# Kernel optimization log

Hardware: AMD Instinct MI355X
Metric: run time of the kernel (lower is better)

The kernel has to match this reference:

```python
import jax, jax.numpy as jnp
import numpy as np

EPS = 1e-7  # K.epsilon()
NUM_ROUTING = 3


def squash(v, axis=-1):
    s = jnp.sum(jnp.square(v), axis=axis, keepdims=True)
    scale = s / (1.0 + s) / jnp.sqrt(s + EPS)
    return scale * v


def setup_inputs() -> dict:
    key = jax.random.key(0)
    k1, k2 = jax.random.split(key)
    B, I, D = 256, 2048, 8      # batch, input_num_capsule, input_dim_capsule
    J, E = 10, 16               # num_capsule, dim_capsule
    inputs = jax.random.normal(k1, (B, I, D), dtype=jnp.float32)
    # glorot-uniform-ish init for W [J, I, E, D]
    limit = np.sqrt(6.0 / (D + E)).astype(np.float32)
    W = jax.random.uniform(k2, (J, I, E, D), dtype=jnp.float32, minval=-limit, maxval=limit)
    return {"inputs": inputs, "W": W}


def reference(inputs, W):
    # u_hat[b,j,i,e] = W[j,i] @ u[b,i]  -> [B, J, I, E]
    u_hat = jnp.einsum('bid,jied->bjie', inputs, W)
    u_hat_stop = jax.lax.stop_gradient(u_hat)
    B, J, I, E = u_hat.shape
    b = jnp.zeros((B, J, I), dtype=u_hat.dtype)
    for i in range(NUM_ROUTING):
        # faithful to tf.nn.softmax(b, dim=1): softmax over num_capsule axis
        c = jax.nn.softmax(b, axis=1)
        if i == NUM_ROUTING - 1:
            outputs = squash(jnp.einsum('bji,bjie->bje', c, u_hat))
        else:
            outputs = squash(jnp.einsum('bji,bjie->bje', c, u_hat_stop))
            b = b + jnp.einsum('bje,bjie->bji', outputs, u_hat_stop)
    # concat along last axis: [B, J, E + I]
    return jnp.concatenate([outputs, c], axis=-1)
```

## Files before the change

### kernel.cpp

```cpp
#include <hip/hip_runtime.h>
#include <math.h>

#define II 2048
#define BB 256
#define JJ 10
#define ICH 16
#define ICHUNKS (II/ICH)
#define SJE (BB*JJ*16)
#define CPAD 20

typedef __attribute__((address_space(3))) unsigned lds_u32;
typedef __attribute__((address_space(1))) const unsigned glb_u32;
typedef _Float16 h4 __attribute__((ext_vector_type(4)));
typedef _Float16 h8 __attribute__((ext_vector_type(8)));
typedef __attribute__((ext_vector_type(4))) float f32x4;

__device__ __forceinline__ void gload16(const void* g, void* l) {
  __builtin_amdgcn_global_load_lds((glb_u32*)g, (lds_u32*)l, 16, 0, 0);
}

template<int N>
__device__ __forceinline__ float rrot16(float v) {
  const int i = __float_as_int(v);
  return __int_as_float(__builtin_amdgcn_update_dpp(i, i, 0x120 + N, 0xF, 0xF, false));
}
__device__ __forceinline__ float rsum16(float v) {
  v += rrot16<8>(v); v += rrot16<4>(v); v += rrot16<2>(v); v += rrot16<1>(v);
  return v;
}
__device__ __forceinline__ float xor16swz(float v) {
  return __int_as_float(__builtin_amdgcn_ds_swizzle(__float_as_int(v), 0x401F));
}

#define XF4 (BB * II * 8 / 4)
#define WF4 (JJ * II * 128 / 4)
__global__ __launch_bounds__(256)
void prep_half(const float* __restrict__ x, const float* __restrict__ W,
               _Float16* __restrict__ xh, _Float16* __restrict__ wh) {
  for (int s = blockIdx.x * 256 + threadIdx.x; s < XF4 + WF4; s += gridDim.x * 256) {
    const float4 v = (s < XF4) ? *reinterpret_cast<const float4*>(x + (size_t)s * 4)
                               : *reinterpret_cast<const float4*>(W + (size_t)(s - XF4) * 4);
    h4 o; o.x = (_Float16)v.x; o.y = (_Float16)v.y; o.z = (_Float16)v.z; o.w = (_Float16)v.w;
    _Float16* dst = (s < XF4) ? (xh + (size_t)s * 4) : (wh + (size_t)(s - XF4) * 4);
    *reinterpret_cast<h4*>(dst) = o;
  }
}

__global__ __launch_bounds__(256)
void pass0_mfma(const _Float16* __restrict__ xh, const _Float16* __restrict__ wh,
                float* __restrict__ part) {
  const int t = threadIdx.x, wid = t >> 6, lane = t & 63;
  const int lg = lane >> 4, lm = lane & 15;
  const int chunk = blockIdx.x * 4 + wid;
  const int mb = blockIdx.y * 16;
  f32x4 acc0 = {0,0,0,0}, acc1 = {0,0,0,0}, acc2 = {0,0,0,0}, acc3 = {0,0,0,0};
  f32x4 acc4_ = {0,0,0,0}, acc5 = {0,0,0,0}, acc6 = {0,0,0,0}, acc7 = {0,0,0,0};
  f32x4 acc8 = {0,0,0,0}, acc9 = {0,0,0,0};
  const int ibase = chunk * 16;
#pragma unroll
  for (int ks = 0; ks < 4; ++ks) {
    const int i = ibase + ks * 4 + lg;
    const h8 a = *reinterpret_cast<const h8*>(xh + ((size_t)(mb + lm) * II + i) * 8);
#define MM(J, ACC)                                                              \
    {                                                                           \
      const h8 bv = *reinterpret_cast<const h8*>(                               \
          wh + (((size_t)(J) * II + i) * 16 + lm) * 8);                         \
      ACC = __builtin_amdgcn_mfma_f32_16x16x32_f16(a, bv, ACC, 0, 0, 0);        \
    }
    MM(0, acc0) MM(1, acc1) MM(2, acc2) MM(3, acc3) MM(4, acc4_)
    MM(5, acc5) MM(6, acc6) MM(7, acc7) MM(8, acc8) MM(9, acc9)
#undef MM
  }
  float* base = part + (size_t)chunk * SJE;
#define ST(J, ACC)                                                        \
  {                                                                       \
    _Pragma("unroll")                                                     \
    for (int r = 0; r < 4; ++r)                                           \
      base[((size_t)(mb + lg * 4 + r) * JJ + (J)) * 16 + lm] = ACC[r];    \
  }
  ST(0, acc0) ST(1, acc1) ST(2, acc2) ST(3, acc3) ST(4, acc4_)
  ST(5, acc5) ST(6, acc6) ST(7, acc7) ST(8, acc8) ST(9, acc9)
#undef ST
}

template<int PASS>
__global__ __launch_bounds__(128, 1)
void routing_mfma(const _Float16* __restrict__ xh, const _Float16* __restrict__ wh,
                  const float* __restrict__ o_eff, float* __restrict__ part,
                  float* __restrict__ out) {
  __shared__ __align__(16) float s_acc[16 * 164];
  __shared__ _Float16 c_tile[(PASS == 2) ? (16 * JJ * CPAD) : 4];

  const int t = threadIdx.x;
  const int w = t >> 6;
  const int lane = t & 63;
  const int lm = lane & 15;
  const int eg = lane >> 4;
  const int ic = blockIdx.x;
  const int b0 = blockIdx.y * 16;
  const int b = b0 + lm;
  const int i0 = ic * ICH;

  float4 o[JJ];
#pragma unroll
  for (int j = 0; j < JJ; ++j)
    o[j] = *reinterpret_cast<const float4*>(
        o_eff + ((size_t)b * JJ + j) * 16 + eg * 4);

  f32x4 acc[JJ];
#pragma unroll
  for (int j = 0; j < JJ; ++j) acc[j] = f32x4{0.f, 0.f, 0.f, 0.f};

  const f32x4 z4 = {0.f, 0.f, 0.f, 0.f};
  h8 xfrag = {0, 0, 0, 0, 0, 0, 0, 0};
  h8 wf[JJ];
#pragma unroll
  for (int j = 0; j < JJ; ++j) wf[j] = h8{0, 0, 0, 0, 0, 0, 0, 0};

  const _Float16* xrow = xh + (size_t)b * II * 8;
  const int ibeg = i0 + w * (ICH / 2);

  if (lane < 16) {
    xfrag = *reinterpret_cast<const h8*>(xrow + (size_t)ibeg * 8);
#pragma unroll
    for (int j = 0; j < JJ; ++j)
      wf[j] = *reinterpret_cast<const h8*>(
          wh + (((size_t)j * II + ibeg) * 16 + lm) * 8);
  }

#pragma unroll 1
  for (int ii = 0; ii < ICH / 2; ++ii) {
    const int i = ibeg + ii;
    const int il = w * (ICH / 2) + ii;
    const int inext = (ii + 1 < ICH / 2) ? (i + 1) : i;

    f32x4 uh[JJ];
#pragma unroll
    for (int j = 0; j < JJ; ++j) {
      uh[j] = __builtin_amdgcn_mfma_f32_16x16x32_f16(wf[j], xfrag, z4, 0, 0, 0);
      if (lane < 16)
        wf[j] = *reinterpret_cast<const h8*>(
            wh + (((size_t)j * II + inext) * 16 + lm) * 8);
    }
    if (lane < 16)
      xfrag = *reinterpret_cast<const h8*>(xrow + (size_t)inext * 8);

    float cj[JJ];
    float D = 0.f;
#pragma unroll
    for (int j = 0; j < JJ; ++j) {
      float v = o[j].x * uh[j][0];
      v = fmaf(o[j].y, uh[j][1], v);
      v = fmaf(o[j].z, uh[j][2], v);
      v = fmaf(o[j].w, uh[j][3], v);
      v += xor16swz(v);
      v += __shfl_xor(v, 32);
      const float pp = __expf(v);
      cj[j] = pp;
      D += pp;
    }
    const float rD = __builtin_amdgcn_rcpf(D);
#pragma unroll
    for (int j = 0; j < JJ; ++j) {
      const float c = cj[j] * rD;
      cj[j] = c;
      acc[j][0] = fmaf(c, uh[j][0], acc[j][0]);
      acc[j][1] = fmaf(c, uh[j][1], acc[j][1]);
      acc[j][2] = fmaf(c, uh[j][2], acc[j][2]);
      acc[j][3] = fmaf(c, uh[j][3], acc[j][3]);
    }
    if (PASS == 2) {
#pragma unroll
      for (int j = 0; j < JJ; ++j) {
        const int owner = (j >= 9) ? 3 : (j / 3);
        if (eg == owner)
          c_tile[(lm * JJ + j) * CPAD + il] = (_Float16)cj[j];
      }
    }
  }

  if (w == 0) {
#pragma unroll
    for (int j = 0; j < JJ; ++j)
      *reinterpret_cast<f32x4*>(&s_acc[lm * 164 + j * 16 + eg * 4]) = acc[j];
  }
  __syncthreads();
  if (w == 1) {
#pragma unroll
    for (int j = 0; j < JJ; ++j) {
      f32x4 v = *reinterpret_cast<const f32x4*>(&s_acc[lm * 164 + j * 16 + eg * 4]);
      v += acc[j];
      *reinterpret_cast<f32x4*>(
          part + (size_t)ic * SJE + ((size_t)b * JJ + j) * 16 + eg * 4) = v;
    }
  }

  if (PASS == 2) {
    for (int s = t; s < 16 * JJ * (ICH / 4); s += 128) {
      const int row = s >> 2, q = s & 3;
      const int bb = row / JJ, jj = row - bb * JJ;
      const h4 cv = *reinterpret_cast<const h4*>(&c_tile[row * CPAD + q * 4]);
      float4 ov;
      ov.x = (float)cv.x; ov.y = (float)cv.y; ov.z = (float)cv.z; ov.w = (float)cv.w;
      *reinterpret_cast<float4*>(
          out + ((size_t)(b0 + bb) * JJ + jj) * 2064 + 16 + i0 + q * 4) = ov;
    }
  }
}

__global__ __launch_bounds__(256)
void finish_pass(const float* __restrict__ part, float* __restrict__ o_eff,
                 float* __restrict__ out, int pass) {
  const int idx = blockIdx.x * 256 + threadIdx.x;
  float a = 0.f;
#pragma unroll 8
  for (int k = 0; k < ICHUNKS; ++k) a += part[(size_t)k * SJE + idx];
  if (pass == 0) a *= 0.1f;
  const float s2 = rsum16(a * a);
  const float scale = s2 / ((1.f + s2) * sqrtf(s2 + 1e-7f));
  const float v = scale * a;
  if (pass == 0) o_eff[idx] = v;
  else if (pass == 1) o_eff[idx] += v;
  else out[(size_t)(idx >> 4) * 2064 + (idx & 15)] = v;
}

#define BBLK 32
#define NBW 8
template<int PASS>
__global__ __launch_bounds__(256, 1)
void routing_pass_atomic(const float* __restrict__ x, const float* __restrict__ W,
                         const float* __restrict__ o_eff, float* __restrict__ sdst,
                         float* __restrict__ out) {
  __shared__ __align__(16) float x_lds[BBLK * ICH * 8];
  __shared__ _Float16 c_tile[(PASS == 2) ? (BBLK * JJ * 18) : 4];

  const int t = threadIdx.x;
  const int wid = t >> 6;
  const int lane = t & 63;
  const int eg = lane >> 4;
  const int j = lane & 15;
  const int jv = (j < JJ);
  const int jr = jv ? j : 0;
  const int ic = blockIdx.x;
  const int b0 = blockIdx.y * BBLK;
  const int bw = __builtin_amdgcn_readfirstlane(b0 + wid * NBW);
  const int i0 = ic * ICH;
  const float* wbase = W + ((size_t)jr * II + i0) * 128 + eg * 32;

  float4 o4[NBW];
  if (PASS > 0) {
#pragma unroll
    for (int nb = 0; nb < NBW; ++nb)
      o4[nb] = *reinterpret_cast<const float4*>(
          o_eff + ((size_t)(bw + nb) * JJ + jr) * 16 + eg * 4);
  }
  float4 acc4[NBW];
#pragma unroll
  for (int nb = 0; nb < NBW; ++nb) acc4[nb] = make_float4(0.f, 0.f, 0.f, 0.f);

#pragma unroll
  for (int k = 0; k < 4; ++k) {
    const int s = k * 256 + t;
    const int bl = s >> 5, rem = s & 31, il = rem >> 1, h = rem & 1;
    gload16(x + ((size_t)(b0 + bl) * II + i0 + il) * 8 + h * 4,
            &x_lds[(k * 256 + wid * 64) * 4]);
  }
  __syncthreads();

#pragma unroll 1
  for (int il = 0; il < ICH; ++il) {
    const float* wp = wbase + il * 128;
    float4 wv[8];
#pragma unroll
    for (int r = 0; r < 8; ++r)
      wv[r] = *reinterpret_cast<const float4*>(wp + r * 4);
#pragma unroll
    for (int nb = 0; nb < NBW; ++nb) {
      const float* xp = &x_lds[((wid * NBW + nb) * ICH + il) * 8];
      const float4 xa = *reinterpret_cast<const float4*>(xp);
      const float4 xb = *reinterpret_cast<const float4*>(xp + 4);
#define DOT8F(q, dst)                                  \
      float dst = wv[2*(q)].x * xa.x;                  \
      dst = fmaf(wv[2*(q)].y, xa.y, dst);              \
      dst = fmaf(wv[2*(q)].z, xa.z, dst);              \
      dst = fmaf(wv[2*(q)].w, xa.w, dst);              \
      dst = fmaf(wv[2*(q)+1].x, xb.x, dst);            \
      dst = fmaf(wv[2*(q)+1].y, xb.y, dst);            \
      dst = fmaf(wv[2*(q)+1].z, xb.z, dst);            \
      dst = fmaf(wv[2*(q)+1].w, xb.w, dst);
      DOT8F(0, u0) DOT8F(1, u1) DOT8F(2, u2) DOT8F(3, u3)
#undef DOT8F
      float c;
      if (PASS == 0) {
        c = 0.1f;
      } else {
        float lp = o4[nb].x * u0;
        lp = fmaf(o4[nb].y, u1, lp);
        lp = fmaf(o4[nb].z, u2, lp);
        lp = fmaf(o4[nb].w, u3, lp);
        lp += xor16swz(lp);
        lp += __shfl_xor(lp, 32);
        const float pp = jv ? __expf(lp) : 0.f;
        const float su = rsum16(pp);
        c = pp * __builtin_amdgcn_rcpf(su);
      }
      acc4[nb].x = fmaf(c, u0, acc4[nb].x);
      acc4[nb].y = fmaf(c, u1, acc4[nb].y);
      acc4[nb].z = fmaf(c, u2, acc4[nb].z);
      acc4[nb].w = fmaf(c, u3, acc4[nb].w);
      if (PASS == 2) {
        if (eg == 0 && jv)
          c_tile[((wid * NBW + nb) * JJ + j) * 18 + il] = (_Float16)c;
      }
    }
  }

  if (PASS == 2) {
    __syncthreads();
    for (int s = t; s < BBLK * JJ * ICH; s += 256) {
      const int row = s >> 4, col = s & 15;
      const int bb = row / 10, jj = row - bb * 10;
      out[((size_t)(b0 + bb) * JJ + jj) * 2064 + 16 + i0 + col] =
          (float)c_tile[row * 18 + col];
    }
  }

  if (jv) {
#pragma unroll
    for (int nb = 0; nb < NBW; ++nb) {
      float* sp = sdst + ((size_t)(bw + nb) * JJ + j) * 16 + eg * 4;
      atomicAdd(&sp[0], acc4[nb].x);
      atomicAdd(&sp[1], acc4[nb].y);
      atomicAdd(&sp[2], acc4[nb].z);
      atomicAdd(&sp[3], acc4[nb].w);
    }
  }
}

__global__ __launch_bounds__(256)
void squash_update(const float* __restrict__ s, float* __restrict__ o_eff,
                   float* __restrict__ out, int pass) {
  const int idx = blockIdx.x * blockDim.x + threadIdx.x;
  if (idx >= BB * JJ) return;
  const float* sp = s + (size_t)idx * 16;
  const float pre = (pass == 0) ? 0.1f : 1.f;
  float v[16];
  float s2 = 0.f;
#pragma unroll
  for (int e = 0; e < 16; ++e) { v[e] = pre * sp[e]; s2 = fmaf(v[e], v[e], s2); }
  const float scale = s2 / ((1.f + s2) * sqrtf(s2 + 1e-7f));
  if (pass == 0) {
    float* op = o_eff + (size_t)idx * 16;
#pragma unroll
    for (int e = 0; e < 16; ++e) op[e] = scale * v[e];
  } else if (pass == 1) {
    float* op = o_eff + (size_t)idx * 16;
#pragma unroll
    for (int e = 0; e < 16; ++e) op[e] += scale * v[e];
  } else {
    float* dst = out + (size_t)idx * 2064;
#pragma unroll
    for (int e = 0; e < 16; ++e) dst[e] = scale * v[e];
  }
}

extern "C" void kernel_launch(void* const* d_in, const int* in_sizes, int n_in,
                              void* d_out, int out_size, void* d_ws, size_t ws_size,
                              hipStream_t stream) {
  const float* x = (const float*)d_in[0];
  const float* W = (const float*)d_in[1];
  float* out = (float*)d_out;
  float* ws = (float*)d_ws;

  const size_t part_f = (size_t)ICHUNKS * SJE;
  const size_t xh_f   = (size_t)BB * II * 8 / 2;
  const size_t wh_f   = (size_t)JJ * II * 128 / 2;
  const size_t need = (part_f + SJE + xh_f + wh_f) * sizeof(float);

  if (ws_size >= need) {
    float* part = ws;
    float* oe   = ws + part_f;
    _Float16* xh = (_Float16*)(ws + part_f + SJE);
    _Float16* wh = (_Float16*)(ws + part_f + SJE + xh_f);
    prep_half<<<2048, 256, 0, stream>>>(x, W, xh, wh);
    pass0_mfma<<<dim3(32, 16), 256, 0, stream>>>(xh, wh, part);
    finish_pass<<<SJE / 256, 256, 0, stream>>>(part, oe, out, 0);
    routing_mfma<1><<<dim3(ICHUNKS, 16), 128, 0, stream>>>(xh, wh, oe, part, nullptr);
    finish_pass<<<SJE / 256, 256, 0, stream>>>(part, oe, out, 1);
    routing_mfma<2><<<dim3(ICHUNKS, 16), 128, 0, stream>>>(xh, wh, oe, part, out);
    finish_pass<<<SJE / 256, 256, 0, stream>>>(part, oe, out, 2);
  } else {
    float* s0 = ws;
    float* s1 = ws + SJE;
    float* s2 = ws + 2 * SJE;
    float* oe = ws + 3 * SJE;
    hipMemsetAsync(ws, 0, (size_t)4 * SJE * sizeof(float), stream);
    routing_pass_atomic<0><<<dim3(ICHUNKS, BB / BBLK), 256, 0, stream>>>(x, W, nullptr, s0, nullptr);
    squash_update<<<10, 256, 0, stream>>>(s0, oe, out, 0);
    routing_pass_atomic<1><<<dim3(ICHUNKS, BB / BBLK), 256, 0, stream>>>(x, W, oe, s1, nullptr);
    squash_update<<<10, 256, 0, stream>>>(s1, oe, out, 1);
    routing_pass_atomic<2><<<dim3(ICHUNKS, BB / BBLK), 256, 0, stream>>>(x, W, oe, s2, out);
    squash_update<<<10, 256, 0, stream>>>(s2, oe, out, 2);
  }
}
```

Measured before the change: 132.1 us.

## Software-pipeline MFMA step against softmax/accumulate of previous capsule

Restructures the per-input-capsule loop into a two-stage software pipeline: the MFMA computing u_hat and the partial agreement logits for step i+1 is issued before the cross-lane reduction, exp, normalization and accumulation of step i. The aim is to hide MFMA and load latency behind VALU/shuffle work. u_hat is kept in fp16 between stages to save registers, which loses precision in the weighted sum. The softmax denominator is also summed as a tree instead of a serial chain.

```diff
diff --git a/kernel.cpp b/kernel.cpp
--- a/kernel.cpp
+++ b/kernel.cpp
@@ -118,7 +118,7 @@
   for (int j = 0; j < JJ; ++j) wf[j] = h8{0, 0, 0, 0, 0, 0, 0, 0};
 
   const _Float16* xrow = xh + (size_t)b * II * 8;
-  const int ibeg = i0 + w * (ICH / 2);
+  const int ibeg = i0 + w * 8;
 
   if (lane < 16) {
     xfrag = *reinterpret_cast<const h8*>(xrow + (size_t)ibeg * 8);
@@ -128,56 +128,76 @@
           wh + (((size_t)j * II + ibeg) * 16 + lm) * 8);
   }
 
+  float lgA[JJ], lgB[JJ];
+  h4 upA[JJ], upB[JJ];
+
+#define MSTEP(LG, UP, INEXT)                                                  \
+  {                                                                           \
+    const int inx_ = (INEXT);                                                 \
+    _Pragma("unroll")                                                         \
+    for (int j = 0; j < JJ; ++j) {                                            \
+      const f32x4 uh_ =                                                       \
+          __builtin_amdgcn_mfma_f32_16x16x32_f16(wf[j], xfrag, z4, 0, 0, 0);  \
+      if (lane < 16)                    \
+        wf[j] = *reinterpret_cast<const h8*>(                                 \
+            wh + (((size_t)j * II + inx_) * 16 + lm) * 8);                    \
+      float v_ = o[j].x * uh_[0];                                             \
+      v_ = fmaf(o[j].y, uh_[1], v_);                                          \
+      v_ = fmaf(o[j].z, uh_[2], v_);                                          \
+      v_ = fmaf(o[j].w, uh_[3], v_);                                          \
+      LG[j] = v_;                                                             \
+      h4 u_;                                                                  \
+      u_.x = (_Float16)uh_[0]; u_.y = (_Float16)uh_[1];                       \
+      u_.z = (_Float16)uh_[2]; u_.w = (_Float16)uh_[3];                       \
+      UP[j] = u_;                                                             \
+    }                                                                         \
+    if (lane < 16)               \
+      xfrag = *reinterpret_cast<const h8*>(xrow + (size_t)inx_ * 8);          \
+  }
+
+#define SSTEP(LG, UP, IL)                                                     \
+  {                                                                           \
+    float p_[JJ];                                                             \
+    _Pragma("unroll")                                                         \
+    for (int j = 0; j < JJ; ++j) {                                            \
+      float v_ = LG[j];                                                       \
+      v_ += xor16swz(v_);                                                     \
+      v_ += __shfl_xor(v_, 32);                                               \
+      p_[j] = __expf(v_);          \
+    }                                                                         \
+    const float d01_ = p_[0] + p_[1], d23_ = p_[2] + p_[3];                   \
+    const float d45_ = p_[4] + p_[5], d67_ = p_[6] + p_[7];                   \
+    const float d89_ = p_[8] + p_[9];                                         \
+    const float D_ = (d01_ + d23_) + (d45_ + d67_) + d89_;                    \
+    const float rD_ = __builtin_amdgcn_rcpf(D_);                              \
+    _Pragma("unroll")                                                         \
+    for (int j = 0; j < JJ; ++j) {                                            \
+      const float c_ = p_[j] * rD_;                                           \
+      acc[j][0] = fmaf(c_, (float)UP[j].x, acc[j][0]);                        \
+      acc[j][1] = fmaf(c_, (float)UP[j].y, acc[j][1]);                        \
+      acc[j][2] = fmaf(c_, (float)UP[j].z, acc[j][2]);                        \
+      acc[j][3] = fmaf(c_, (float)UP[j].w, acc[j][3]);                        \
+      if (PASS == 2) {                                                        \
+        const int owner_ = (j >= 9) ? 3 : (j / 3);                            \
+        if (eg == owner_)                                                     \
+          c_tile[(lm * JJ + j) * CPAD + (IL)] = (_Float16)c_;                 \
+      }                                                                       \
+    }                                                                         \
+  }
+
+  MSTEP(lgA, upA, ibeg + 1)
 #pragma unroll 1
-  for (int ii = 0; ii < ICH / 2; ++ii) {
-    const int i = ibeg + ii;
-    const int il = w * (ICH / 2) + ii;
-    const int inext = (ii + 1 < ICH / 2) ? (i + 1) : i;
-
-    f32x4 uh[JJ];
-#pragma unroll
-    for (int j = 0; j < JJ; ++j) {
-      uh[j] = __builtin_amdgcn_mfma_f32_16x16x32_f16(wf[j], xfrag, z4, 0, 0, 0);
-      if (lane < 16)
-        wf[j] = *reinterpret_cast<const h8*>(
-            wh + (((size_t)j * II + inext) * 16 + lm) * 8);
-    }
-    if (lane < 16)
-      xfrag = *reinterpret_cast<const h8*>(xrow + (size_t)inext * 8);
-
-    float cj[JJ];
-    float D = 0.f;
-#pragma unroll
-    for (int j = 0; j < JJ; ++j) {
-      float v = o[j].x * uh[j][0];
-      v = fmaf(o[j].y, uh[j][1], v);
-      v = fmaf(o[j].z, uh[j][2], v);
-      v = fmaf(o[j].w, uh[j][3], v);
-      v += xor16swz(v);
-      v += __shfl_xor(v, 32);
-      const float pp = __expf(v);
-      cj[j] = pp;
-      D += pp;
-    }
-    const float rD = __builtin_amdgcn_rcpf(D);
-#pragma unroll
-    for (int j = 0; j < JJ; ++j) {
-      const float c = cj[j] * rD;
-      cj[j] = c;
-      acc[j][0] = fmaf(c, uh[j][0], acc[j][0]);
-      acc[j][1] = fmaf(c, uh[j][1], acc[j][1]);
-      acc[j][2] = fmaf(c, uh[j][2], acc[j][2]);
-      acc[j][3] = fmaf(c, uh[j][3], acc[j][3]);
-    }
-    if (PASS == 2) {
-#pragma unroll
-      for (int j = 0; j < JJ; ++j) {
-        const int owner = (j >= 9) ? 3 : (j / 3);
-        if (eg == owner)
-          c_tile[(lm * JJ + j) * CPAD + il] = (_Float16)cj[j];
-      }
-    }
-  }
+  for (int k = 0; k < 3; ++k) {
+    MSTEP(lgB, upB, ibeg + 2 * k + 2)
+    SSTEP(lgA, upA, w * 8 + 2 * k)
+    MSTEP(lgA, upA, ibeg + 2 * k + 3)
+    SSTEP(lgB, upB, w * 8 + 2 * k + 1)
+  }
+  MSTEP(lgB, upB, ibeg + 7)
+  SSTEP(lgA, upA, w * 8 + 6)
+  SSTEP(lgB, upB, w * 8 + 7)
+#undef MSTEP
+#undef SSTEP
 
   if (w == 0) {
 #pragma unroll
```

Result: no change. 133.6 us (+1.1%).

## Stage routing outputs in LDS, pack u_hat to fp16, load fragments on all lanes

Applied to the files above, without the earlier changes.

The per-thread o_eff vectors move from registers into a shared-memory tile, and u_hat values are held as fp16 between the logit and accumulation phases. This cuts register pressure and drops the min-blocks launch bound, so more waves can be resident per CU. W and x fragments are now loaded on all lanes without the lane<16 predicate, which replicates the K dimension and scales u_hat by four. That factor is compensated with 0.25 scaling on o and in finish_pass. The risks are fp16 rounding of u_hat in the accumulation, extra redundant global loads, and extra LDS reads inside the loop.

```diff
diff --git a/kernel.cpp b/kernel.cpp
--- a/kernel.cpp
+++ b/kernel.cpp
@@ -84,11 +84,11 @@
 }
 
 template<int PASS>
-__global__ __launch_bounds__(128, 1)
+__global__ __launch_bounds__(128)
 void routing_mfma(const _Float16* __restrict__ xh, const _Float16* __restrict__ wh,
                   const float* __restrict__ o_eff, float* __restrict__ part,
                   float* __restrict__ out) {
-  __shared__ __align__(16) float s_acc[16 * 164];
+  __shared__ __align__(16) float ols[16 * 164];
   __shared__ _Float16 c_tile[(PASS == 2) ? (16 * JJ * CPAD) : 4];
 
   const int t = threadIdx.x;
@@ -101,94 +101,99 @@
   const int b = b0 + lm;
   const int i0 = ic * ICH;
 
-  float4 o[JJ];
+  for (int s = t; s < 640; s += 128) {
+    const int bb = s / 40, rem = s - bb * 40;
+    const float4 v = *reinterpret_cast<const float4*>(
+        o_eff + (size_t)(b0 + bb) * 160 + rem * 4);
+    float4 sv;
+    sv.x = 0.25f * v.x; sv.y = 0.25f * v.y; sv.z = 0.25f * v.z; sv.w = 0.25f * v.w;
+    *reinterpret_cast<float4*>(&ols[bb * 164 + rem * 4]) = sv;
+  }
+  __syncthreads();
+
+  f32x4 acc[JJ];
+#pragma unroll
+  for (int j = 0; j < JJ; ++j) acc[j] = f32x4{0.f, 0.f, 0.f, 0.f};
+
+  const f32x4 z4 = {0.f, 0.f, 0.f, 0.f};
+  const _Float16* wp = wh + lm * 8;
+  const _Float16* xp = xh + (size_t)b * II * 8;
+  const int ibeg = i0 + w * 8;
+
+  h8 wf[JJ];
+  h8 xf;
 #pragma unroll
   for (int j = 0; j < JJ; ++j)
-    o[j] = *reinterpret_cast<const float4*>(
-        o_eff + ((size_t)b * JJ + j) * 16 + eg * 4);
-
-  f32x4 acc[JJ];
-#pragma unroll
-  for (int j = 0; j < JJ; ++j) acc[j] = f32x4{0.f, 0.f, 0.f, 0.f};
-
-  const f32x4 z4 = {0.f, 0.f, 0.f, 0.f};
-  h8 xfrag = {0, 0, 0, 0, 0, 0, 0, 0};
-  h8 wf[JJ];
-#pragma unroll
-  for (int j = 0; j < JJ; ++j) wf[j] = h8{0, 0, 0, 0, 0, 0, 0, 0};
-
-  const _Float16* xrow = xh + (size_t)b * II * 8;
-  const int ibeg = i0 + w * (ICH / 2);
-
-  if (lane < 16) {
-    xfrag = *reinterpret_cast<const h8*>(xrow + (size_t)ibeg * 8);
+    wf[j] = *reinterpret_cast<const h8*>(wp + ((size_t)j * II + ibeg) * 128);
+  xf = *reinterpret_cast<const h8*>(xp + (size_t)ibeg * 8);
+
+#pragma unroll 1
+  for (int ii = 0; ii < 8; ++ii) {
+    const int il = w * 8 + ii;
+    const int inx = ibeg + ((ii < 7) ? ii + 1 : ii);
+
+    float lg[JJ];
+    h4 up[JJ];
+#pragma unroll
+    for (int j = 0; j < JJ; ++j) {
+      const f32x4 uhj =
+          __builtin_amdgcn_mfma_f32_16x16x32_f16(wf[j], xf, z4, 0, 0, 0);
+      const float4 o4 = *reinterpret_cast<const float4*>(
+          &ols[lm * 164 + j * 16 + eg * 4]);
+      float v = o4.x * uhj[0];
+      v = fmaf(o4.y, uhj[1], v);
+      v = fmaf(o4.z, uhj[2], v);
+      v = fmaf(o4.w, uhj[3], v);
+      lg[j] = v;
+      h4 u; u.x = (_Float16)uhj[0]; u.y = (_Float16)uhj[1];
+      u.z = (_Float16)uhj[2]; u.w = (_Float16)uhj[3];
+      up[j] = u;
+    }
+
 #pragma unroll
     for (int j = 0; j < JJ; ++j)
-      wf[j] = *reinterpret_cast<const h8*>(
-          wh + (((size_t)j * II + ibeg) * 16 + lm) * 8);
-  }
-
-#pragma unroll 1
-  for (int ii = 0; ii < ICH / 2; ++ii) {
-    const int i = ibeg + ii;
-    const int il = w * (ICH / 2) + ii;
-    const int inext = (ii + 1 < ICH / 2) ? (i + 1) : i;
-
-    f32x4 uh[JJ];
+      wf[j] = *reinterpret_cast<const h8*>(wp + ((size_t)j * II + inx) * 128);
+    xf = *reinterpret_cast<const h8*>(xp + (size_t)inx * 8);
+
+    float p[JJ];
 #pragma unroll
     for (int j = 0; j < JJ; ++j) {
-      uh[j] = __builtin_amdgcn_mfma_f32_16x16x32_f16(wf[j], xfrag, z4, 0, 0, 0);
-      if (lane < 16)
-        wf[j] = *reinterpret_cast<const h8*>(
-            wh + (((size_t)j * II + inext) * 16 + lm) * 8);
-    }
-    if (lane < 16)
-      xfrag = *reinterpret_cast<const h8*>(xrow + (size_t)inext * 8);
-
-    float cj[JJ];
-    float D = 0.f;
-#pragma unroll
-    for (int j = 0; j < JJ; ++j) {
-      float v = o[j].x * uh[j][0];
-      v = fmaf(o[j].y, uh[j][1], v);
-      v = fmaf(o[j].z, uh[j][2], v);
-      v = fmaf(o[j].w, uh[j][3], v);
+      float v = lg[j];
       v += xor16swz(v);
       v += __shfl_xor(v, 32);
-      const float pp = __expf(v);
-      cj[j] = pp;
-      D += pp;
-    }
+      p[j] = __expf(v);
+    }
+    const float d01 = p[0] + p[1], d23 = p[2] + p[3];
+    const float d45 = p[4] + p[5], d67 = p[6] + p[7];
+    const float d89 = p[8] + p[9];
+    const float D = (d01 + d23) + (d45 + d67) + d89;
     const float rD = __builtin_amdgcn_rcpf(D);
 #pragma unroll
     for (int j = 0; j < JJ; ++j) {
-      const float c = cj[j] * rD;
-      cj[j] = c;
-      acc[j][0] = fmaf(c, uh[j][0], acc[j][0]);
-      acc[j][1] = fmaf(c, uh[j][1], acc[j][1]);
-      acc[j][2] = fmaf(c, uh[j][2], acc[j][2]);
-      acc[j][3] = fmaf(c, uh[j][3], acc[j][3]);
-    }
-    if (PASS == 2) {
-#pragma unroll
-      for (int j = 0; j < JJ; ++j) {
+      const float c = p[j] * rD;
+      acc[j][0] = fmaf(c, (float)up[j].x, acc[j][0]);
+      acc[j][1] = fmaf(c, (float)up[j].y, acc[j][1]);
+      acc[j][2] = fmaf(c, (float)up[j].z, acc[j][2]);
+      acc[j][3] = fmaf(c, (float)up[j].w, acc[j][3]);
+      if (PASS == 2) {
         const int owner = (j >= 9) ? 3 : (j / 3);
         if (eg == owner)
-          c_tile[(lm * JJ + j) * CPAD + il] = (_Float16)cj[j];
+          c_tile[(lm * JJ + j) * CPAD + il] = (_Float16)c;
       }
     }
   }
 
+  __syncthreads();
   if (w == 0) {
 #pragma unroll
     for (int j = 0; j < JJ; ++j)
-      *reinterpret_cast<f32x4*>(&s_acc[lm * 164 + j * 16 + eg * 4]) = acc[j];
+      *reinterpret_cast<f32x4*>(&ols[lm * 164 + j * 16 + eg * 4]) = acc[j];
   }
   __syncthreads();
   if (w == 1) {
 #pragma unroll
     for (int j = 0; j < JJ; ++j) {
-      f32x4 v = *reinterpret_cast<const f32x4*>(&s_acc[lm * 164 + j * 16 + eg * 4]);
+      f32x4 v = *reinterpret_cast<const f32x4*>(&ols[lm * 164 + j * 16 + eg * 4]);
       v += acc[j];
       *reinterpret_cast<f32x4*>(
           part + (size_t)ic * SJE + ((size_t)b * JJ + j) * 16 + eg * 4) = v;
@@ -215,7 +220,7 @@
   float a = 0.f;
 #pragma unroll 8
   for (int k = 0; k < ICHUNKS; ++k) a += part[(size_t)k * SJE + idx];
-  if (pass == 0) a *= 0.1f;
+  a *= (pass == 0) ? 0.1f : 0.25f;
   const float s2 = rsum16(a * a);
   const float scale = s2 / ((1.f + s2) * sqrtf(s2 + 1e-7f));
   const float v = scale * a;
```

After: 114.4 us. 1.15x faster.
